# Kernel tuning notes

Hardware: AMD Instinct MI355X
Metric: run time of the kernel (lower is better)

## Reference

```python
import jax, jax.numpy as jnp
import numpy as np
import math

D_MODEL = 1024
N_HEADS = 16
D_K = D_MODEL // N_HEADS


def setup_inputs() -> dict:
    key = jax.random.key(0)
    ks = jax.random.split(key, 5)
    std = math.sqrt(2.0 / (D_MODEL + D_MODEL))
    x = jax.random.normal(ks[0], (2, 2048, D_MODEL), dtype=jnp.float32)
    W_q = jax.random.normal(ks[1], (D_MODEL, D_MODEL), dtype=jnp.float32) * std
    W_k = jax.random.normal(ks[2], (D_MODEL, D_MODEL), dtype=jnp.float32) * std
    W_v = jax.random.normal(ks[3], (D_MODEL, D_MODEL), dtype=jnp.float32) * std
    W_o = jax.random.normal(ks[4], (D_MODEL, D_MODEL), dtype=jnp.float32) * std
    return {"x": x, "W_q": W_q, "W_k": W_k, "W_v": W_v, "W_o": W_o}


def reference(x, W_q, W_k, W_v, W_o):
    B, S, D = x.shape
    H, dk = N_HEADS, D_K
    # projections: (B,S,D) @ (D,D)
    def split_heads(t):  # (B,S,D) -> (B,H,S,dk)
        return t.reshape(B, S, H, dk).transpose(0, 2, 1, 3)
    Q = split_heads(x @ W_q)
    K = split_heads(x @ W_k)
    V = split_heads(x @ W_v)
    scale = 1.0 / math.sqrt(dk)
    scores = jnp.einsum("bhqd,bhkd->bhqk", Q, K) * scale  # (B,H,S,S)
    attn = jax.nn.softmax(scores, axis=-1)
    out = jnp.einsum("bhqk,bhkd->bhqd", attn, V)  # (B,H,S,dk)
    concat = out.transpose(0, 2, 1, 3).reshape(B, S, D)
    return concat @ W_o
```

## Files before the change

kernel.cpp:

```cpp
#include <hip/hip_runtime.h>
#include <hip/hip_bf16.h>
#include <math.h>

#define DMODEL 1024
#define NHEADS 16
#define DKH    64
#define BATCH  2
#define SEQ    2048
#define MROWS  (BATCH * SEQ)
#define LOG2E  1.4426950408889634f

typedef __bf16 bf16_t;
typedef bf16_t bf16x8 __attribute__((ext_vector_type(8)));
typedef bf16_t bf16x4 __attribute__((ext_vector_type(4)));
typedef float  floatx4 __attribute__((ext_vector_type(4)));

__device__ __forceinline__ void glds16(const bf16_t* g, bf16_t* l) {
    __builtin_amdgcn_global_load_lds((__attribute__((address_space(1))) unsigned*)(g),
                                     (__attribute__((address_space(3))) unsigned*)(l),
                                     16, 0, 0);
}

__global__ void prep_kernel(const float* __restrict__ x,
                            const float* __restrict__ W0, const float* __restrict__ W1,
                            const float* __restrict__ W2, const float* __restrict__ W3,
                            bf16_t* __restrict__ xb, bf16_t* __restrict__ Wt) {
    __shared__ float t[32][33];
    int bx = blockIdx.x, by = blockIdx.y, z = blockIdx.z;
    int tx = threadIdx.x, ty = threadIdx.y;
    if (z == 0) {
        int tid = ty * 32 + tx;
#pragma unroll
        for (int k = 0; k < 4; ++k) {
            int slot = k * 256 + tid;
            int row = by * 128 + (slot >> 3);
            int col = bx * 32 + (slot & 7) * 4;
            float4 v = *(const float4*)&x[(size_t)row * DMODEL + col];
            bf16x4 o = {(bf16_t)v.x, (bf16_t)v.y, (bf16_t)v.z, (bf16_t)v.w};
            *(bf16x4*)&xb[(size_t)row * DMODEL + col] = o;
        }
        return;
    }
    const float* W = (z == 1) ? W0 : (z == 2) ? W1 : (z == 3) ? W2 : W3;
    bf16_t* dst = Wt + (size_t)(z - 1) * DMODEL * DMODEL;
#pragma unroll
    for (int i = 0; i < 32; i += 8)
        t[ty + i][tx] = W[(size_t)(by * 32 + ty + i) * DMODEL + bx * 32 + tx];
    __syncthreads();
#pragma unroll
    for (int i = 0; i < 32; i += 8)
        dst[(size_t)(bx * 32 + ty + i) * DMODEL + by * 32 + tx] = (bf16_t)t[tx][ty + i];
}

__global__ __launch_bounds__(256) void gemm_qkv_kernel(const bf16_t* __restrict__ A,
                                                       const bf16_t* __restrict__ Bt,
                                                       bf16_t* __restrict__ Qfb,
                                                       bf16_t* __restrict__ Kfb,
                                                       bf16_t* __restrict__ Vfb) {
    __shared__ bf16_t sm[16384];
    bf16_t* As = sm;
    bf16_t* Bs = sm + 8192;
    int tid = threadIdx.x;
    int w = tid >> 6, l = tid & 63, g = l >> 4, lm = l & 15;
    int wr = w >> 1, wc = w & 1;
    int m0 = blockIdx.y * 128, n0 = blockIdx.x * 128;
    int r8 = l >> 3, s8 = l & 7, cw = s8 ^ r8;

    floatx4 acc[4][4];
#pragma unroll
    for (int i = 0; i < 4; ++i)
#pragma unroll
        for (int j = 0; j < 4; ++j) { floatx4 z = {0.f, 0.f, 0.f, 0.f}; acc[i][j] = z; }

    const bf16_t* Ag = A  + (size_t)(m0 + w * 32 + r8) * DMODEL + cw * 8;
    const bf16_t* Bg = Bt + (size_t)(n0 + w * 32 + r8) * DMODEL + cw * 8;

    for (int k0 = 0; k0 < DMODEL; k0 += 64) {
        __syncthreads();
#pragma unroll
        for (int j = 0; j < 4; ++j) {
            glds16(Ag + (size_t)j * 8 * DMODEL + k0, &As[(w * 32 + j * 8) * 64]);
            glds16(Bg + (size_t)j * 8 * DMODEL + k0, &Bs[(w * 32 + j * 8) * 64]);
        }
        __syncthreads();
#pragma unroll
        for (int kk = 0; kk < 2; ++kk) {
            bf16x8 af[4], bfr[4];
            int c = kk * 4 + g;
            int sw = (c ^ (lm & 7)) * 8;
#pragma unroll
            for (int i = 0; i < 4; ++i) {
                af[i]  = *(const bf16x8*)&As[(wr * 64 + i * 16 + lm) * 64 + sw];
                bfr[i] = *(const bf16x8*)&Bs[(wc * 64 + i * 16 + lm) * 64 + sw];
            }
#pragma unroll
            for (int i = 0; i < 4; ++i)
#pragma unroll
                for (int j = 0; j < 4; ++j)
                    acc[i][j] = __builtin_amdgcn_mfma_f32_16x16x32_bf16(af[i], bfr[j], acc[i][j], 0, 0, 0);
        }
    }

    __syncthreads();
    int mat = n0 >> 10;
    int headb = (n0 & 1023) >> 6;
    int b = m0 >> 11;
    int ktb = (m0 & 2047) >> 6;
    float scale = (mat == 0) ? (0.125f * LOG2E) : 1.0f;

    if (mat <= 1) {
#pragma unroll
        for (int i = 0; i < 4; ++i)
#pragma unroll
            for (int j = 0; j < 4; ++j) {
                int d = j * 16 + lm;
                int base = (wc * 2 + wr) * 4096 + (i * 2 + (d >> 5)) * 512 + ((d >> 3) & 3) * 128 + (d & 7);
#pragma unroll
                for (int r = 0; r < 4; ++r)
                    sm[base + (g * 4 + r) * 8] = (bf16_t)(acc[i][j][r] * scale);
            }
    } else {
#pragma unroll
        for (int i = 0; i < 4; ++i)
#pragma unroll
            for (int j = 0; j < 4; ++j) {
                int base = (wc * 2 + wr) * 4096 + (j * 2 + (i >> 1)) * 512 +
                           (((i & 1) * 2 + (g >> 1)) * 16 + lm) * 8 + (g & 1) * 4;
                bf16x4 pk = {(bf16_t)acc[i][j][0], (bf16_t)acc[i][j][1],
                             (bf16_t)acc[i][j][2], (bf16_t)acc[i][j][3]};
                *(bf16x4*)&sm[base] = pk;
            }
    }
    __syncthreads();
    bf16_t* outbuf = (mat == 0) ? Qfb : (mat == 1) ? Kfb : Vfb;
#pragma unroll
    for (int rep = 0; rep < 8; ++rep) {
        int idx = rep * 256 + tid;
        int c = idx >> 9;
        int off = (idx & 511) * 8;
        int bh2 = b * NHEADS + headb + (c >> 1);
        int kt = ktb + (c & 1);
        *(bf16x8*)(outbuf + ((size_t)bh2 * 32 + kt) * 4096 + off) = *(const bf16x8*)&sm[c * 4096 + off];
    }
}

__global__ __launch_bounds__(256) void gemmO_kernel(const bf16_t* __restrict__ A,
                                                    const bf16_t* __restrict__ Bt,
                                                    float* __restrict__ outp) {
    __shared__ bf16_t As[64 * 64];
    __shared__ bf16_t Bs[128 * 64];
    int tid = threadIdx.x;
    int w = tid >> 6, l = tid & 63, g = l >> 4, lm = l & 15;
    int wr = w & 1, wc = w >> 1;
    int m0 = blockIdx.y * 64, n0 = blockIdx.x * 128;
    int r8 = l >> 3, s8 = l & 7, cw = s8 ^ r8;

    floatx4 acc[2][4];
#pragma unroll
    for (int i = 0; i < 2; ++i)
#pragma unroll
        for (int j = 0; j < 4; ++j) { floatx4 z = {0.f, 0.f, 0.f, 0.f}; acc[i][j] = z; }

    const bf16_t* Ag = A  + (size_t)(m0 + w * 16 + r8) * DMODEL + cw * 8;
    const bf16_t* Bg = Bt + (size_t)(n0 + w * 32 + r8) * DMODEL + cw * 8;

    for (int k0 = 0; k0 < DMODEL; k0 += 64) {
        __syncthreads();
#pragma unroll
        for (int j = 0; j < 2; ++j)
            glds16(Ag + (size_t)j * 8 * DMODEL + k0, &As[(w * 16 + j * 8) * 64]);
#pragma unroll
        for (int j = 0; j < 4; ++j)
            glds16(Bg + (size_t)j * 8 * DMODEL + k0, &Bs[(w * 32 + j * 8) * 64]);
        __syncthreads();
#pragma unroll
        for (int kk = 0; kk < 2; ++kk) {
            bf16x8 af[2], bfr[4];
            int c = kk * 4 + g;
            int sw = (c ^ (lm & 7)) * 8;
#pragma unroll
            for (int i = 0; i < 2; ++i)
                af[i] = *(const bf16x8*)&As[(wr * 32 + i * 16 + lm) * 64 + sw];
#pragma unroll
            for (int j = 0; j < 4; ++j)
                bfr[j] = *(const bf16x8*)&Bs[(wc * 64 + j * 16 + lm) * 64 + sw];
#pragma unroll
            for (int i = 0; i < 2; ++i)
#pragma unroll
                for (int j = 0; j < 4; ++j)
                    acc[i][j] = __builtin_amdgcn_mfma_f32_16x16x32_bf16(af[i], bfr[j], acc[i][j], 0, 0, 0);
        }
    }

#pragma unroll
    for (int i = 0; i < 2; ++i)
#pragma unroll
        for (int j = 0; j < 4; ++j) {
            int nc = n0 + wc * 64 + j * 16 + lm;
            int mb = m0 + wr * 32 + i * 16 + g * 4;
#pragma unroll
            for (int r = 0; r < 4; ++r)
                outp[(size_t)(mb + r) * DMODEL + nc] = acc[i][j][r];
        }
}

__global__ __launch_bounds__(256, 2) void attn_kernel(const bf16_t* __restrict__ Qf,
                                                      const bf16_t* __restrict__ Kf,
                                                      const bf16_t* __restrict__ Vf,
                                                      bf16_t* __restrict__ Cc) {
    __shared__ __align__(16) char smem[24576];
    bf16_t* Ps   = (bf16_t*)smem;
    float*  Mbuf = (float*)smem;
    float*  Lbuf = (float*)(smem + 20480);
    bf16_t* Ct   = (bf16_t*)(smem + 21504);

    int tid = threadIdx.x;
    int w = tid >> 6, l = tid & 63, g = l >> 4, lm = l & 15;
    int bh = blockIdx.x, b = bh >> 4, h = bh & 15;
    int q0 = blockIdx.y * 64;

    const bf16_t* Qfh = Qf + ((size_t)bh * 32 + (q0 >> 6)) * 4096 + l * 8;
    const bf16_t* Kfh = Kf + (size_t)bh * 32 * 4096 + l * 8;
    const bf16_t* Vfh = Vf + (size_t)bh * 32 * 4096 + l * 8;

    bf16x8 qf[4][2];
#pragma unroll
    for (int nt = 0; nt < 4; ++nt)
#pragma unroll
        for (int kk = 0; kk < 2; ++kk)
            qf[nt][kk] = *(const bf16x8*)(Qfh + (nt * 2 + kk) * 512);

    floatx4 oacc[4][4];
#pragma unroll
    for (int dt = 0; dt < 4; ++dt)
#pragma unroll
        for (int nt = 0; nt < 4; ++nt) { floatx4 z = {0.f, 0.f, 0.f, 0.f}; oacc[dt][nt] = z; }
    float lsum[4] = {0.f, 0.f, 0.f, 0.f};

    int kt0 = w * 8;
    bf16x8 kfa[2][2], kfb[2][2], vfa[4], vfb[4];
    {
        const bf16_t* Kb0 = Kfh + (size_t)kt0 * 4096;
#pragma unroll
        for (int m2 = 0; m2 < 2; ++m2)
#pragma unroll
            for (int kk = 0; kk < 2; ++kk)
                kfa[m2][kk] = *(const bf16x8*)(Kb0 + (m2 * 2 + kk) * 512);
    }

    for (int it = 0; it < 8; ++it) {
        const bf16_t* Tb = Kfh + (size_t)(kt0 + it) * 4096;
        const bf16_t* Vb = Vfh + (size_t)(kt0 + it) * 4096;
        const bf16_t* Tn = Kfh + (size_t)(kt0 + ((it < 7) ? it + 1 : 0)) * 4096;

#pragma unroll
        for (int dt = 0; dt < 4; ++dt) vfa[dt] = *(const bf16x8*)(Vb + (dt * 2 + 0) * 512);
#pragma unroll
        for (int m2 = 0; m2 < 2; ++m2)
#pragma unroll
            for (int kk = 0; kk < 2; ++kk)
                kfb[m2][kk] = *(const bf16x8*)(Tb + (4 + m2 * 2 + kk) * 512);

        floatx4 sa[2][4];
#pragma unroll
        for (int m2 = 0; m2 < 2; ++m2)
#pragma unroll
            for (int nt = 0; nt < 4; ++nt) { floatx4 z = {0.f, 0.f, 0.f, 0.f}; sa[m2][nt] = z; }
        __builtin_amdgcn_s_setprio(1);
#pragma unroll
        for (int kk = 0; kk < 2; ++kk)
#pragma unroll
            for (int m2 = 0; m2 < 2; ++m2)
#pragma unroll
                for (int nt = 0; nt < 4; ++nt)
                    sa[m2][nt] = __builtin_amdgcn_mfma_f32_16x16x32_bf16(kfa[m2][kk], qf[nt][kk], sa[m2][nt], 0, 0, 0);
        __builtin_amdgcn_s_setprio(0);

#pragma unroll
        for (int dt = 0; dt < 4; ++dt) vfb[dt] = *(const bf16x8*)(Vb + (dt * 2 + 1) * 512);
#pragma unroll
        for (int m2 = 0; m2 < 2; ++m2)
#pragma unroll
            for (int kk = 0; kk < 2; ++kk)
                kfa[m2][kk] = *(const bf16x8*)(Tn + (m2 * 2 + kk) * 512);

        floatx4 sb[2][4];
#pragma unroll
        for (int m2 = 0; m2 < 2; ++m2)
#pragma unroll
            for (int nt = 0; nt < 4; ++nt) { floatx4 z = {0.f, 0.f, 0.f, 0.f}; sb[m2][nt] = z; }
        __builtin_amdgcn_s_setprio(1);
#pragma unroll
        for (int kk = 0; kk < 2; ++kk)
#pragma unroll
            for (int m2 = 0; m2 < 2; ++m2)
#pragma unroll
                for (int nt = 0; nt < 4; ++nt)
                    sb[m2][nt] = __builtin_amdgcn_mfma_f32_16x16x32_bf16(kfb[m2][kk], qf[nt][kk], sb[m2][nt], 0, 0, 0);
        __builtin_amdgcn_s_setprio(0);

#pragma unroll
        for (int m2 = 0; m2 < 2; ++m2)
#pragma unroll
            for (int nt = 0; nt < 4; ++nt) {
                float p0 = __builtin_amdgcn_exp2f(sa[m2][nt][0]);
                float p1 = __builtin_amdgcn_exp2f(sa[m2][nt][1]);
                float p2 = __builtin_amdgcn_exp2f(sa[m2][nt][2]);
                float p3 = __builtin_amdgcn_exp2f(sa[m2][nt][3]);
                lsum[nt] += (p0 + p1) + (p2 + p3);
                bf16x4 pk = {(bf16_t)p0, (bf16_t)p1, (bf16_t)p2, (bf16_t)p3};
                *(bf16x4*)&Ps[w * 2560 + (nt * 16 + lm) * 40 + m2 * 16 + g * 4] = pk;
            }
        {
            bf16x8 bp[4];
#pragma unroll
            for (int nt = 0; nt < 4; ++nt)
                bp[nt] = *(const bf16x8*)&Ps[w * 2560 + (nt * 16 + lm) * 40 + g * 8];
            __builtin_amdgcn_s_setprio(1);
#pragma unroll
            for (int dt = 0; dt < 4; ++dt)
#pragma unroll
                for (int nt = 0; nt < 4; ++nt)
                    oacc[dt][nt] = __builtin_amdgcn_mfma_f32_16x16x32_bf16(vfa[dt], bp[nt], oacc[dt][nt], 0, 0, 0);
            __builtin_amdgcn_s_setprio(0);
        }

#pragma unroll
        for (int m2 = 0; m2 < 2; ++m2)
#pragma unroll
            for (int nt = 0; nt < 4; ++nt) {
                float p0 = __builtin_amdgcn_exp2f(sb[m2][nt][0]);
                float p1 = __builtin_amdgcn_exp2f(sb[m2][nt][1]);
                float p2 = __builtin_amdgcn_exp2f(sb[m2][nt][2]);
                float p3 = __builtin_amdgcn_exp2f(sb[m2][nt][3]);
                lsum[nt] += (p0 + p1) + (p2 + p3);
                bf16x4 pk = {(bf16_t)p0, (bf16_t)p1, (bf16_t)p2, (bf16_t)p3};
                *(bf16x4*)&Ps[w * 2560 + (nt * 16 + lm) * 40 + m2 * 16 + g * 4] = pk;
            }
        {
            bf16x8 bp[4];
#pragma unroll
            for (int nt = 0; nt < 4; ++nt)
                bp[nt] = *(const bf16x8*)&Ps[w * 2560 + (nt * 16 + lm) * 40 + g * 8];
            __builtin_amdgcn_s_setprio(1);
#pragma unroll
            for (int dt = 0; dt < 4; ++dt)
#pragma unroll
                for (int nt = 0; nt < 4; ++nt)
                    oacc[dt][nt] = __builtin_amdgcn_mfma_f32_16x16x32_bf16(vfb[dt], bp[nt], oacc[dt][nt], 0, 0, 0);
            __builtin_amdgcn_s_setprio(0);
        }
    }

#pragma unroll
    for (int nt = 0; nt < 4; ++nt) {
        float s = lsum[nt];
        s += __shfl_xor(s, 16, 64);
        s += __shfl_xor(s, 32, 64);
        lsum[nt] = s;
    }

    float linv = 0.f;
#pragma unroll
    for (int p = 0; p < 4; ++p) {
        __syncthreads();
#pragma unroll
        for (int nt = 0; nt < 4; ++nt)
            *(floatx4*)&Mbuf[w * 1280 + (nt * 16 + lm) * 20 + g * 4] = oacc[p][nt];
        if (p == 0 && g == 0)
#pragma unroll
            for (int nt = 0; nt < 4; ++nt)
                Lbuf[w * 64 + nt * 16 + lm] = lsum[nt];
        __syncthreads();
        if (p == 0) {
            float lt = 0.f;
#pragma unroll
            for (int w2 = 0; w2 < 4; ++w2)
                lt += Lbuf[w2 * 64 + w * 16 + lm];
            linv = 1.0f / lt;
        }
        {
            floatx4 s = {0.f, 0.f, 0.f, 0.f};
#pragma unroll
            for (int w2 = 0; w2 < 4; ++w2)
                s += *(const floatx4*)&Mbuf[w2 * 1280 + (w * 16 + lm) * 20 + g * 4];
            bf16x4 pk = {(bf16_t)(s[0] * linv), (bf16_t)(s[1] * linv),
                         (bf16_t)(s[2] * linv), (bf16_t)(s[3] * linv)};
            *(bf16x4*)&Ct[w * 384 + lm * 24 + g * 4] = pk;
        }
        {
            int row = l >> 2, dp = l & 3;
            bf16x4 v = *(const bf16x4*)&Ct[w * 384 + row * 24 + dp * 4];
            *(bf16x4*)&Cc[((size_t)(b * SEQ + q0 + w * 16 + row)) * DMODEL + h * DKH + p * 16 + dp * 4] = v;
        }
    }
}

extern "C" void kernel_launch(void* const* d_in, const int* in_sizes, int n_in,
                              void* d_out, int out_size, void* d_ws, size_t ws_size,
                              hipStream_t stream) {
    const float* x  = (const float*)d_in[0];
    const float* Wq = (const float*)d_in[1];
    const float* Wk = (const float*)d_in[2];
    const float* Wv = (const float*)d_in[3];
    const float* Wo = (const float*)d_in[4];

    const size_t NX = (size_t)MROWS * DMODEL;
    const size_t NW = (size_t)DMODEL * DMODEL;
    bf16_t* ws  = (bf16_t*)d_ws;
    bf16_t* xb  = ws;
    bf16_t* Wt  = xb + NX;
    bf16_t* Wto = Wt + 3 * NW;
    bf16_t* Qfb = Wt + 4 * NW;
    bf16_t* Kfb = Qfb + NX;
    bf16_t* Vfb = Kfb + NX;
    bf16_t* Cc  = Vfb + NX;

    prep_kernel<<<dim3(32, 32, 5), dim3(32, 8), 0, stream>>>(x, Wq, Wk, Wv, Wo, xb, Wt);

    gemm_qkv_kernel<<<dim3(3 * DMODEL / 128, MROWS / 128), 256, 0, stream>>>(xb, Wt, Qfb, Kfb, Vfb);

    attn_kernel<<<dim3(BATCH * NHEADS, SEQ / 64), 256, 0, stream>>>(Qfb, Kfb, Vfb, Cc);

    gemmO_kernel<<<dim3(DMODEL / 128, MROWS / 64), 256, 0, stream>>>(Cc, Wto, (float*)d_out);
}
```

Before: 178.3 us.

## Permute K fragment layout so P stays in registers, dropping LDS round-trip

```diff
diff --git a/kernel.cpp b/kernel.cpp
--- a/kernel.cpp
+++ b/kernel.cpp
@@ -106,9 +106,9 @@
     int headb = (n0 & 1023) >> 6;
     int b = m0 >> 11;
     int ktb = (m0 & 2047) >> 6;
-    float scale = (mat == 0) ? (0.125f * LOG2E) : 1.0f;
-
-    if (mat <= 1) {
+
+    if (mat == 0) {
+        const float scale = 0.125f * LOG2E;
 #pragma unroll
         for (int i = 0; i < 4; ++i)
 #pragma unroll
@@ -118,6 +118,18 @@
 #pragma unroll
                 for (int r = 0; r < 4; ++r)
                     sm[base + (g * 4 + r) * 8] = (bf16_t)(acc[i][j][r] * scale);
+            }
+    } else if (mat == 1) {
+#pragma unroll
+        for (int i = 0; i < 4; ++i)
+#pragma unroll
+            for (int j = 0; j < 4; ++j) {
+                int d = j * 16 + lm;
+                int base = (wc * 2 + wr) * 4096 + ((i >> 1) * 4 + (g & 1) * 2 + (d >> 5)) * 512 +
+                           ((d >> 3) & 3) * 128 + ((i & 1) * 8 + (g >> 1) * 4) * 8 + (d & 7);
+#pragma unroll
+                for (int r = 0; r < 4; ++r)
+                    sm[base + r * 8] = (bf16_t)acc[i][j][r];
             }
     } else {
 #pragma unroll
@@ -209,7 +221,6 @@
                                                       const bf16_t* __restrict__ Vf,
                                                       bf16_t* __restrict__ Cc) {
     __shared__ __align__(16) char smem[24576];
-    bf16_t* Ps   = (bf16_t*)smem;
     float*  Mbuf = (float*)smem;
     float*  Lbuf = (float*)(smem + 20480);
     bf16_t* Ct   = (bf16_t*)(smem + 21504);
@@ -242,10 +253,10 @@
     {
         const bf16_t* Kb0 = Kfh + (size_t)kt0 * 4096;
 #pragma unroll
-        for (int m2 = 0; m2 < 2; ++m2)
+        for (int c = 0; c < 2; ++c)
 #pragma unroll
             for (int kk = 0; kk < 2; ++kk)
-                kfa[m2][kk] = *(const bf16x8*)(Kb0 + (m2 * 2 + kk) * 512);
+                kfa[c][kk] = *(const bf16x8*)(Kb0 + (c * 2 + kk) * 512);
     }
 
     for (int it = 0; it < 8; ++it) {
@@ -256,66 +267,66 @@
 #pragma unroll
         for (int dt = 0; dt < 4; ++dt) vfa[dt] = *(const bf16x8*)(Vb + (dt * 2 + 0) * 512);
 #pragma unroll
-        for (int m2 = 0; m2 < 2; ++m2)
+        for (int c = 0; c < 2; ++c)
 #pragma unroll
             for (int kk = 0; kk < 2; ++kk)
-                kfb[m2][kk] = *(const bf16x8*)(Tb + (4 + m2 * 2 + kk) * 512);
+                kfb[c][kk] = *(const bf16x8*)(Tb + (4 + c * 2 + kk) * 512);
 
         floatx4 sa[2][4];
 #pragma unroll
-        for (int m2 = 0; m2 < 2; ++m2)
-#pragma unroll
-            for (int nt = 0; nt < 4; ++nt) { floatx4 z = {0.f, 0.f, 0.f, 0.f}; sa[m2][nt] = z; }
+        for (int c = 0; c < 2; ++c)
+#pragma unroll
+            for (int nt = 0; nt < 4; ++nt) { floatx4 z = {0.f, 0.f, 0.f, 0.f}; sa[c][nt] = z; }
         __builtin_amdgcn_s_setprio(1);
 #pragma unroll
         for (int kk = 0; kk < 2; ++kk)
 #pragma unroll
-            for (int m2 = 0; m2 < 2; ++m2)
+            for (int c = 0; c < 2; ++c)
 #pragma unroll
                 for (int nt = 0; nt < 4; ++nt)
-                    sa[m2][nt] = __builtin_amdgcn_mfma_f32_16x16x32_bf16(kfa[m2][kk], qf[nt][kk], sa[m2][nt], 0, 0, 0);
+                    sa[c][nt] = __builtin_amdgcn_mfma_f32_16x16x32_bf16(kfa[c][kk], qf[nt][kk], sa[c][nt], 0, 0, 0);
         __builtin_amdgcn_s_setprio(0);
 
 #pragma unroll
         for (int dt = 0; dt < 4; ++dt) vfb[dt] = *(const bf16x8*)(Vb + (dt * 2 + 1) * 512);
 #pragma unroll
-        for (int m2 = 0; m2 < 2; ++m2)
+        for (int c = 0; c < 2; ++c)
 #pragma unroll
             for (int kk = 0; kk < 2; ++kk)
-                kfa[m2][kk] = *(const bf16x8*)(Tn + (m2 * 2 + kk) * 512);
+                kfa[c][kk] = *(const bf16x8*)(Tn + (c * 2 + kk) * 512);
 
         floatx4 sb[2][4];
 #pragma unroll
-        for (int m2 = 0; m2 < 2; ++m2)
-#pragma unroll
-            for (int nt = 0; nt < 4; ++nt) { floatx4 z = {0.f, 0.f, 0.f, 0.f}; sb[m2][nt] = z; }
+        for (int c = 0; c < 2; ++c)
+#pragma unroll
+            for (int nt = 0; nt < 4; ++nt) { floatx4 z = {0.f, 0.f, 0.f, 0.f}; sb[c][nt] = z; }
         __builtin_amdgcn_s_setprio(1);
 #pragma unroll
         for (int kk = 0; kk < 2; ++kk)
 #pragma unroll
-            for (int m2 = 0; m2 < 2; ++m2)
+            for (int c = 0; c < 2; ++c)
 #pragma unroll
                 for (int nt = 0; nt < 4; ++nt)
-                    sb[m2][nt] = __builtin_amdgcn_mfma_f32_16x16x32_bf16(kfb[m2][kk], qf[nt][kk], sb[m2][nt], 0, 0, 0);
+                    sb[c][nt] = __builtin_amdgcn_mfma_f32_16x16x32_bf16(kfb[c][kk], qf[nt][kk], sb[c][nt], 0, 0, 0);
         __builtin_amdgcn_s_setprio(0);
 
-#pragma unroll
-        for (int m2 = 0; m2 < 2; ++m2)
-#pragma unroll
-            for (int nt = 0; nt < 4; ++nt) {
-                float p0 = __builtin_amdgcn_exp2f(sa[m2][nt][0]);
-                float p1 = __builtin_amdgcn_exp2f(sa[m2][nt][1]);
-                float p2 = __builtin_amdgcn_exp2f(sa[m2][nt][2]);
-                float p3 = __builtin_amdgcn_exp2f(sa[m2][nt][3]);
-                lsum[nt] += (p0 + p1) + (p2 + p3);
-                bf16x4 pk = {(bf16_t)p0, (bf16_t)p1, (bf16_t)p2, (bf16_t)p3};
-                *(bf16x4*)&Ps[w * 2560 + (nt * 16 + lm) * 40 + m2 * 16 + g * 4] = pk;
-            }
         {
             bf16x8 bp[4];
 #pragma unroll
-            for (int nt = 0; nt < 4; ++nt)
-                bp[nt] = *(const bf16x8*)&Ps[w * 2560 + (nt * 16 + lm) * 40 + g * 8];
+            for (int nt = 0; nt < 4; ++nt) {
+                float p0 = __builtin_amdgcn_exp2f(sa[0][nt][0]);
+                float p1 = __builtin_amdgcn_exp2f(sa[0][nt][1]);
+                float p2 = __builtin_amdgcn_exp2f(sa[0][nt][2]);
+                float p3 = __builtin_amdgcn_exp2f(sa[0][nt][3]);
+                float p4 = __builtin_amdgcn_exp2f(sa[1][nt][0]);
+                float p5 = __builtin_amdgcn_exp2f(sa[1][nt][1]);
+                float p6 = __builtin_amdgcn_exp2f(sa[1][nt][2]);
+                float p7 = __builtin_amdgcn_exp2f(sa[1][nt][3]);
+                lsum[nt] += ((p0 + p1) + (p2 + p3)) + ((p4 + p5) + (p6 + p7));
+                bf16x8 pk = {(bf16_t)p0, (bf16_t)p1, (bf16_t)p2, (bf16_t)p3,
+                             (bf16_t)p4, (bf16_t)p5, (bf16_t)p6, (bf16_t)p7};
+                bp[nt] = pk;
+            }
             __builtin_amdgcn_s_setprio(1);
 #pragma unroll
             for (int dt = 0; dt < 4; ++dt)
@@ -325,23 +336,23 @@
             __builtin_amdgcn_s_setprio(0);
         }
 
-#pragma unroll
-        for (int m2 = 0; m2 < 2; ++m2)
-#pragma unroll
-            for (int nt = 0; nt < 4; ++nt) {
-                float p0 = __builtin_amdgcn_exp2f(sb[m2][nt][0]);
-                float p1 = __builtin_amdgcn_exp2f(sb[m2][nt][1]);
-                float p2 = __builtin_amdgcn_exp2f(sb[m2][nt][2]);
-                float p3 = __builtin_amdgcn_exp2f(sb[m2][nt][3]);
-                lsum[nt] += (p0 + p1) + (p2 + p3);
-                bf16x4 pk = {(bf16_t)p0, (bf16_t)p1, (bf16_t)p2, (bf16_t)p3};
-                *(bf16x4*)&Ps[w * 2560 + (nt * 16 + lm) * 40 + m2 * 16 + g * 4] = pk;
-            }
         {
             bf16x8 bp[4];
 #pragma unroll
-            for (int nt = 0; nt < 4; ++nt)
-                bp[nt] = *(const bf16x8*)&Ps[w * 2560 + (nt * 16 + lm) * 40 + g * 8];
+            for (int nt = 0; nt < 4; ++nt) {
+                float p0 = __builtin_amdgcn_exp2f(sb[0][nt][0]);
+                float p1 = __builtin_amdgcn_exp2f(sb[0][nt][1]);
+                float p2 = __builtin_amdgcn_exp2f(sb[0][nt][2]);
+                float p3 = __builtin_amdgcn_exp2f(sb[0][nt][3]);
+                float p4 = __builtin_amdgcn_exp2f(sb[1][nt][0]);
+                float p5 = __builtin_amdgcn_exp2f(sb[1][nt][1]);
+                float p6 = __builtin_amdgcn_exp2f(sb[1][nt][2]);
+                float p7 = __builtin_amdgcn_exp2f(sb[1][nt][3]);
+                lsum[nt] += ((p0 + p1) + (p2 + p3)) + ((p4 + p5) + (p6 + p7));
+                bf16x8 pk = {(bf16_t)p0, (bf16_t)p1, (bf16_t)p2, (bf16_t)p3,
+                             (bf16_t)p4, (bf16_t)p5, (bf16_t)p6, (bf16_t)p7};
+                bp[nt] = pk;
+            }
             __builtin_amdgcn_s_setprio(1);
 #pragma unroll
             for (int dt = 0; dt < 4; ++dt)
```

Result: faster. 173.3 us (-2.8%).
